# Kernel tuning notes

Hardware: AMD Instinct MI355X
Metric: run time of the kernel (lower is better)

The kernel has to match this reference:

```python
import jax, jax.numpy as jnp
import numpy as np

IMAGE_SIZE = 512


def _build_masks(image_size):
    # Vectorized equivalent of the module's triple-loop pyramid construction.
    w = h = image_size
    x = w - 1  # pyramid is (w-1, h-1)
    idx = np.arange(x)
    J, K = np.meshgrid(idx, idx, indexing='ij')
    # ring index i at (j,k) is min distance to any border of the (x,x) square
    ring = np.minimum(np.minimum(J, K), np.minimum(x - 1 - J, x - 1 - K))
    pyramid = x // 2 - ring
    plane = np.full((w, h), w // 2, dtype=np.int64)
    plane[1:, 1:] = pyramid
    L = image_size // 2 + 1  # number of bins
    # one-hot rectangular-ring masks: mask[r] = (plane == r)
    mask = (plane[None, :, :] == np.arange(L)[:, None, None]).astype(np.float32)
    mask_n = np.maximum(mask.sum(axis=(1, 2)), 1e-8).astype(np.float32)
    return jnp.asarray(mask), jnp.asarray(mask_n)


def setup_inputs() -> dict:
    key = jax.random.key(0)
    x = jax.random.uniform(key, (16, 3, IMAGE_SIZE, IMAGE_SIZE), dtype=jnp.float32)
    mask, mask_n = _build_masks(IMAGE_SIZE)
    return {"x": x, "mask": mask, "mask_n": mask_n}


def reference(x, mask, mask_n):
    # only_psd=True branch: RGB -> luma, scaled by 20
    mag = 20.0 * (0.299 * x[:, 0] + 0.587 * x[:, 1] + 0.114 * x[:, 2])  # [B,H,W]
    # per-bin masked average; einsum avoids materializing [B,L,H,W]
    profile = jnp.einsum('bhw,lhw->bl', mag, mask) / mask_n  # [B,L]
    pmin = profile.min()
    pmax = profile.max()
    return (profile - pmin) / (pmax - pmin)
```

## Files before the change

### kernel.cpp

```cpp
#include <hip/hip_runtime.h>

#define IMG 512
#define HW (IMG * IMG)
#define NB 257
#define BATCH 16


__global__ __launch_bounds__(256) void hist_kernel(const float* __restrict__ x,
                                                   float* __restrict__ prof) {
    const int b    = blockIdx.y;
    const int wid  = threadIdx.x >> 6;
    const int lane = threadIdx.x & 63;
    const int h    = (blockIdx.x << 2) + wid;

    __shared__ float bins[NB];
    for (int i = threadIdx.x; i < NB; i += 256) bins[i] = 0.f;
    __syncthreads();

    const float* xr  = x + (size_t)b * 3 * HW + (size_t)h * IMG;
    const float* xg  = xr + HW;
    const float* xbl = xg + HW;

    const int m = min(h - 1, 511 - h);
    float mid = 0.f;

#pragma unroll
    for (int j = 0; j < 2; ++j) {
        const int w0 = (((j << 6) + lane) << 2);
        const float4 r  = *reinterpret_cast<const float4*>(xr  + w0);
        const float4 g  = *reinterpret_cast<const float4*>(xg  + w0);
        const float4 bv = *reinterpret_cast<const float4*>(xbl + w0);

        float mg[4];
        mg[0] = 20.f * (0.299f * r.x + 0.587f * g.x + 0.114f * bv.x);
        mg[1] = 20.f * (0.299f * r.y + 0.587f * g.y + 0.114f * bv.y);
        mg[2] = 20.f * (0.299f * r.z + 0.587f * g.z + 0.114f * bv.z);
        mg[3] = 20.f * (0.299f * r.w + 0.587f * g.w + 0.114f * bv.w);

        if (h == 0) {
            mid += mg[0] + mg[1] + mg[2] + mg[3];
        } else {
#pragma unroll
            for (int t = 0; t < 4; ++t) {
                const int w = w0 + t;
                if (w == 0) {
                    atomicAdd(&bins[256], mg[t]);
                } else {
                    const int d = min(w - 1, 511 - w);
                    if (d >= m) mid += mg[t];
                    else        atomicAdd(&bins[255 - d], mg[t]);
                }
            }
        }
    }

#pragma unroll
    for (int off = 32; off > 0; off >>= 1) mid += __shfl_down(mid, off, 64);
    if (lane == 0) atomicAdd(&bins[(h == 0) ? 256 : (255 - m)], mid);
    __syncthreads();

    float* pb = prof + (size_t)b * NB;
    for (int i = threadIdx.x; i < NB; i += 256) {
        const float v = bins[i];
        if (v != 0.f) atomicAdd(&pb[i], v);
    }
}

__global__ __launch_bounds__(256) void finalize_kernel(const float* __restrict__ prof,
                                                       const float* __restrict__ mask_n,
                                                       float* __restrict__ out) {
    __shared__ float smin[256];
    __shared__ float smax[256];
    float lmin = 3.402823466e+38f, lmax = -3.402823466e+38f;
    for (int i = threadIdx.x; i < BATCH * NB; i += 256) {
        const float v = prof[i] / mask_n[i % NB];
        lmin = fminf(lmin, v);
        lmax = fmaxf(lmax, v);
    }
    smin[threadIdx.x] = lmin;
    smax[threadIdx.x] = lmax;
    __syncthreads();
    for (int s = 128; s > 0; s >>= 1) {
        if (threadIdx.x < s) {
            smin[threadIdx.x] = fminf(smin[threadIdx.x], smin[threadIdx.x + s]);
            smax[threadIdx.x] = fmaxf(smax[threadIdx.x], smax[threadIdx.x + s]);
        }
        __syncthreads();
    }
    const float pmin = smin[0];
    const float inv = 1.f / (smax[0] - pmin);
    for (int i = threadIdx.x; i < BATCH * NB; i += 256) {
        const float v = prof[i] / mask_n[i % NB];
        out[i] = (v - pmin) * inv;
    }
}

extern "C" void kernel_launch(void* const* d_in, const int* in_sizes, int n_in,
                              void* d_out, int out_size, void* d_ws, size_t ws_size,
                              hipStream_t stream) {
    const float* x      = (const float*)d_in[0];
    const float* mask_n = (const float*)d_in[2];
    float* out  = (float*)d_out;
    float* prof = (float*)d_ws;

    hipMemsetAsync(prof, 0, (size_t)BATCH * NB * sizeof(float), stream);
    hist_kernel<<<dim3(128, BATCH), 256, 0, stream>>>(x, prof);
    finalize_kernel<<<1, 256, 0, stream>>>(prof, mask_n, out);
}
```

Measured before the change: 42.35 us.

## Replace global atomics and memset with per-block partial histograms reduced in finalize

Each hist block now handles 16 rows (4 per wave) instead of 4 and writes its shared-memory bins to a private partial slot, removing the memset launch and the global atomicAdds. The finalize kernel uses 1024 threads, sums the 32 partials per bin, caches the profile in shared memory, and does the min/max with wave shuffles. This cuts launch count and atomic contention, but it reduces the hist grid from 2048 to 512 blocks and moves more serial summing into the single-block finalize.

```diff
diff --git a/kernel.cpp b/kernel.cpp
--- a/kernel.cpp
+++ b/kernel.cpp
@@ -4,95 +4,109 @@
 #define HW (IMG * IMG)
 #define NB 257
 #define BATCH 16
+#define RG 32
 
 
 __global__ __launch_bounds__(256) void hist_kernel(const float* __restrict__ x,
-                                                   float* __restrict__ prof) {
+                                                   float* __restrict__ partial) {
+    const int gx   = blockIdx.x;
     const int b    = blockIdx.y;
     const int wid  = threadIdx.x >> 6;
     const int lane = threadIdx.x & 63;
-    const int h    = (blockIdx.x << 2) + wid;
 
     __shared__ float bins[NB];
     for (int i = threadIdx.x; i < NB; i += 256) bins[i] = 0.f;
     __syncthreads();
 
-    const float* xr  = x + (size_t)b * 3 * HW + (size_t)h * IMG;
-    const float* xg  = xr + HW;
-    const float* xbl = xg + HW;
-
-    const int m = min(h - 1, 511 - h);
-    float mid = 0.f;
+    const float* xbase = x + (size_t)b * 3 * HW;
+    const int h0 = (gx << 4) + (wid << 2);
 
 #pragma unroll
-    for (int j = 0; j < 2; ++j) {
-        const int w0 = (((j << 6) + lane) << 2);
-        const float4 r  = *reinterpret_cast<const float4*>(xr  + w0);
-        const float4 g  = *reinterpret_cast<const float4*>(xg  + w0);
-        const float4 bv = *reinterpret_cast<const float4*>(xbl + w0);
+    for (int rr = 0; rr < 4; ++rr) {
+        const int h = h0 + rr;
+        const float* xr  = xbase + (size_t)h * IMG;
+        const float* xg  = xr + HW;
+        const float* xbl = xg + HW;
+        const int m = min(h - 1, 511 - h);
+        float mid = 0.f;
+#pragma unroll
+        for (int j = 0; j < 2; ++j) {
+            const int w0 = (((j << 6) + lane) << 2);
+            const float4 r  = *reinterpret_cast<const float4*>(xr  + w0);
+            const float4 g  = *reinterpret_cast<const float4*>(xg  + w0);
+            const float4 bv = *reinterpret_cast<const float4*>(xbl + w0);
+            float mg[4];
+            mg[0] = 20.f * (0.299f * r.x + 0.587f * g.x + 0.114f * bv.x);
+            mg[1] = 20.f * (0.299f * r.y + 0.587f * g.y + 0.114f * bv.y);
+            mg[2] = 20.f * (0.299f * r.z + 0.587f * g.z + 0.114f * bv.z);
+            mg[3] = 20.f * (0.299f * r.w + 0.587f * g.w + 0.114f * bv.w);
 
-        float mg[4];
-        mg[0] = 20.f * (0.299f * r.x + 0.587f * g.x + 0.114f * bv.x);
-        mg[1] = 20.f * (0.299f * r.y + 0.587f * g.y + 0.114f * bv.y);
-        mg[2] = 20.f * (0.299f * r.z + 0.587f * g.z + 0.114f * bv.z);
-        mg[3] = 20.f * (0.299f * r.w + 0.587f * g.w + 0.114f * bv.w);
-
-        if (h == 0) {
-            mid += mg[0] + mg[1] + mg[2] + mg[3];
-        } else {
+            if (h == 0) {
+                mid += mg[0] + mg[1] + mg[2] + mg[3];
+            } else {
 #pragma unroll
-            for (int t = 0; t < 4; ++t) {
-                const int w = w0 + t;
-                if (w == 0) {
-                    atomicAdd(&bins[256], mg[t]);
-                } else {
-                    const int d = min(w - 1, 511 - w);
-                    if (d >= m) mid += mg[t];
-                    else        atomicAdd(&bins[255 - d], mg[t]);
+                for (int t = 0; t < 4; ++t) {
+                    const int w = w0 + t;
+                    if (w == 0) {
+                        atomicAdd(&bins[256], mg[t]);
+                    } else {
+                        const int d = min(w - 1, 511 - w);
+                        if (d >= m) mid += mg[t];
+                        else        atomicAdd(&bins[255 - d], mg[t]);
+                    }
                 }
             }
         }
+#pragma unroll
+        for (int off = 32; off > 0; off >>= 1) mid += __shfl_down(mid, off, 64);
+        if (lane == 0) atomicAdd(&bins[(h == 0) ? 256 : (255 - m)], mid);
     }
-
-#pragma unroll
-    for (int off = 32; off > 0; off >>= 1) mid += __shfl_down(mid, off, 64);
-    if (lane == 0) atomicAdd(&bins[(h == 0) ? 256 : (255 - m)], mid);
     __syncthreads();
 
-    float* pb = prof + (size_t)b * NB;
-    for (int i = threadIdx.x; i < NB; i += 256) {
-        const float v = bins[i];
-        if (v != 0.f) atomicAdd(&pb[i], v);
-    }
+    float* pp = partial + ((size_t)b * RG + gx) * NB;
+    for (int i = threadIdx.x; i < NB; i += 256) pp[i] = bins[i];
 }
 
-__global__ __launch_bounds__(256) void finalize_kernel(const float* __restrict__ prof,
-                                                       const float* __restrict__ mask_n,
-                                                       float* __restrict__ out) {
-    __shared__ float smin[256];
-    __shared__ float smax[256];
+__global__ __launch_bounds__(1024) void finalize_kernel(const float* __restrict__ partial,
+                                                        const float* __restrict__ mask_n,
+                                                        float* __restrict__ out) {
+    __shared__ float prof_s[BATCH * NB];
+    __shared__ float red_min[16];
+    __shared__ float red_max[16];
+
+    const int lane = threadIdx.x & 63;
+    const int wv   = threadIdx.x >> 6;
+
     float lmin = 3.402823466e+38f, lmax = -3.402823466e+38f;
-    for (int i = threadIdx.x; i < BATCH * NB; i += 256) {
-        const float v = prof[i] / mask_n[i % NB];
-        lmin = fminf(lmin, v);
-        lmax = fmaxf(lmax, v);
+    for (int i = threadIdx.x; i < BATCH * NB; i += 1024) {
+        const int bb = i / NB;
+        const int l  = i - bb * NB;
+        const float* p = partial + (size_t)bb * RG * NB + l;
+        float s = 0.f;
+#pragma unroll
+        for (int g = 0; g < RG; ++g) s += p[(size_t)g * NB];
+        s /= mask_n[l];
+        prof_s[i] = s;
+        lmin = fminf(lmin, s);
+        lmax = fmaxf(lmax, s);
     }
-    smin[threadIdx.x] = lmin;
-    smax[threadIdx.x] = lmax;
+#pragma unroll
+    for (int off = 32; off > 0; off >>= 1) {
+        lmin = fminf(lmin, __shfl_xor(lmin, off, 64));
+        lmax = fmaxf(lmax, __shfl_xor(lmax, off, 64));
+    }
+    if (lane == 0) { red_min[wv] = lmin; red_max[wv] = lmax; }
     __syncthreads();
-    for (int s = 128; s > 0; s >>= 1) {
-        if (threadIdx.x < s) {
-            smin[threadIdx.x] = fminf(smin[threadIdx.x], smin[threadIdx.x + s]);
-            smax[threadIdx.x] = fmaxf(smax[threadIdx.x], smax[threadIdx.x + s]);
-        }
-        __syncthreads();
+
+    float pmin = red_min[0], pmax = red_max[0];
+#pragma unroll
+    for (int k = 1; k < 16; ++k) {
+        pmin = fminf(pmin, red_min[k]);
+        pmax = fmaxf(pmax, red_max[k]);
     }
-    const float pmin = smin[0];
-    const float inv = 1.f / (smax[0] - pmin);
-    for (int i = threadIdx.x; i < BATCH * NB; i += 256) {
-        const float v = prof[i] / mask_n[i % NB];
-        out[i] = (v - pmin) * inv;
-    }
+    const float inv = 1.f / (pmax - pmin);
+    for (int i = threadIdx.x; i < BATCH * NB; i += 1024)
+        out[i] = (prof_s[i] - pmin) * inv;
 }
 
 extern "C" void kernel_launch(void* const* d_in, const int* in_sizes, int n_in,
@@ -100,10 +114,9 @@
                               hipStream_t stream) {
     const float* x      = (const float*)d_in[0];
     const float* mask_n = (const float*)d_in[2];
-    float* out  = (float*)d_out;
-    float* prof = (float*)d_ws;
+    float* out     = (float*)d_out;
+    float* partial = (float*)d_ws;
 
-    hipMemsetAsync(prof, 0, (size_t)BATCH * NB * sizeof(float), stream);
-    hist_kernel<<<dim3(128, BATCH), 256, 0, stream>>>(x, prof);
-    finalize_kernel<<<1, 256, 0, stream>>>(prof, mask_n, out);
+    hist_kernel<<<dim3(RG, BATCH), 256, 0, stream>>>(x, partial);
+    finalize_kernel<<<1, 1024, 0, stream>>>(partial, mask_n, out);
 }
```

Measured after the change: 38.75 us. 8.5% less time.
